# Kernel tuning notes

Measured on AMD Instinct MI355X. Metric: run time of the kernel, lower is better.

The kernel has to match this reference:

```python
import jax, jax.numpy as jnp
import numpy as np

B = 2_000_000
INPUT_DIM = 2
HIDDEN = 32
HALF = HIDDEN // 2  # 16
N_BUCKETS = 50


def setup_inputs() -> dict:
    key = jax.random.key(0)
    ks = jax.random.split(key, 8)
    x = jax.random.normal(ks[0], (B, INPUT_DIM), dtype=jnp.float32)
    buckets = jax.random.randint(ks[1], (B,), 0, N_BUCKETS)
    # shared MLP params (Linear stores W as [out,in]; we keep [in,out] for einsum)
    W1 = jax.random.normal(ks[2], (INPUT_DIM, HIDDEN), dtype=jnp.float32) * 0.5
    b1 = jax.random.normal(ks[3], (HIDDEN,), dtype=jnp.float32) * 0.1
    W2 = jax.random.normal(ks[4], (HIDDEN, HALF), dtype=jnp.float32) * 0.2
    b2 = jax.random.normal(ks[5], (HALF,), dtype=jnp.float32) * 0.1
    # per-bucket heads: each Linear(HALF, 1) -> stacked [N_BUCKETS, HALF] + [N_BUCKETS]
    Wh = jax.random.normal(ks[6], (N_BUCKETS, HALF), dtype=jnp.float32) * 0.2
    bh = jax.random.normal(ks[7], (N_BUCKETS,), dtype=jnp.float32) * 0.1
    return {"x": x, "buckets": buckets, "W1": W1, "b1": b1, "W2": W2, "b2": b2, "Wh": Wh, "bh": bh}


def reference(x, buckets, W1, b1, W2, b2, Wh, bh):
    # shared MLP: Linear -> ReLU -> Linear
    h = jax.nn.relu(x @ W1 + b1) @ W2 + b2            # [B, HALF]
    # bucket routing with clamp-to-last for out-of-range ids
    ids = jnp.where(buckets < N_BUCKETS, buckets, N_BUCKETS - 1)  # [B]
    w = Wh[ids]                                        # [B, HALF] gather
    out = jnp.einsum('bd,bd->b', h, w) + bh[ids]       # [B]
    return out
```

## Files before the change

### kernel.cpp

```cpp
#include <hip/hip_runtime.h>

#define NB 50
#define BLOCK 256


__global__ __launch_bounds__(BLOCK) void precompute_kernel(
    const float* __restrict__ W2,
    const float* __restrict__ b2,
    const float* __restrict__ Wh,
    const float* __restrict__ bh,
    float*       __restrict__ ws)
{
    int t = blockIdx.x * BLOCK + threadIdx.x;
    if (t < NB * 32) {
        int id = t >> 5;
        int k  = t & 31;
        float s = 0.f;
        #pragma unroll
        for (int j = 0; j < 16; ++j)
            s = fmaf(W2[(k << 4) + j], Wh[(id << 4) + j], s);
        int h = (id + (id >> 3)) & 7;
        ws[(id << 5) | ((((k >> 2) ^ h) & 7) << 2) | (k & 3)] = s;
    } else if (t < NB * 32 + NB) {
        int id = t - NB * 32;
        float s = bh[id];
        #pragma unroll
        for (int j = 0; j < 16; ++j)
            s = fmaf(b2[j], Wh[(id << 4) + j], s);
        ws[NB * 32 + id] = s;
    }
}

__device__ __forceinline__ float dot4relu(float x0, float x1,
                                          float4 wa, float4 wb, float4 bb,
                                          float4 v, float acc)
{
    float h;
    h = fmaf(x0, wa.x, fmaf(x1, wb.x, bb.x)); h = fmaxf(h, 0.f); acc = fmaf(h, v.x, acc);
    h = fmaf(x0, wa.y, fmaf(x1, wb.y, bb.y)); h = fmaxf(h, 0.f); acc = fmaf(h, v.y, acc);
    h = fmaf(x0, wa.z, fmaf(x1, wb.z, bb.z)); h = fmaxf(h, 0.f); acc = fmaf(h, v.z, acc);
    h = fmaf(x0, wa.w, fmaf(x1, wb.w, bb.w)); h = fmaxf(h, 0.f); acc = fmaf(h, v.w, acc);
    return acc;
}

__global__ __launch_bounds__(BLOCK) void lightwin_kernel(
    const float4* __restrict__ xq,
    const int4*   __restrict__ bq,
    const float*  __restrict__ W1,
    const float*  __restrict__ b1,
    const float4* __restrict__ wsq,
    float4*       __restrict__ outq,
    int nq)
{
    __shared__ float sVc[416 * 4];

    int tid = blockIdx.x * BLOCK + threadIdx.x;
    bool active = tid < nq;

    float4 xa = {}, xb = {};
    int4 ib = {};
    if (active) {
        xa = xq[2 * tid];
        xb = xq[2 * tid + 1];
        ib = bq[tid];
    }

    float4* sq = (float4*)sVc;
    #pragma unroll
    for (int t = threadIdx.x; t < 416; t += BLOCK)
        sq[t] = wsq[t];
    __syncthreads();

    if (!active) return;

    int id0 = ib.x < NB ? ib.x : NB - 1;
    int id1 = ib.y < NB ? ib.y : NB - 1;
    int id2 = ib.z < NB ? ib.z : NB - 1;
    int id3 = ib.w < NB ? ib.w : NB - 1;
    int h0 = (id0 + (id0 >> 3)) & 7;
    int h1 = (id1 + (id1 >> 3)) & 7;
    int h2 = (id2 + (id2 >> 3)) & 7;
    int h3 = (id3 + (id3 >> 3)) & 7;

    const float4* sV4 = (const float4*)sVc;
    const float*  sc  = sVc + NB * 32;
    const float4* W14 = (const float4*)W1;
    const float4* b14 = (const float4*)b1;

    float acc0 = sc[id0];
    float acc1 = sc[id1];
    float acc2 = sc[id2];
    float acc3 = sc[id3];

    #pragma unroll
    for (int kb = 0; kb < 8; ++kb) {
        float4 wa = W14[kb];
        float4 wb = W14[8 + kb];
        float4 bb = b14[kb];
        float4 v0 = sV4[(id0 << 3) | ((kb ^ h0) & 7)];
        float4 v1 = sV4[(id1 << 3) | ((kb ^ h1) & 7)];
        float4 v2 = sV4[(id2 << 3) | ((kb ^ h2) & 7)];
        float4 v3 = sV4[(id3 << 3) | ((kb ^ h3) & 7)];
        acc0 = dot4relu(xa.x, xa.y, wa, wb, bb, v0, acc0);
        acc1 = dot4relu(xa.z, xa.w, wa, wb, bb, v1, acc1);
        acc2 = dot4relu(xb.x, xb.y, wa, wb, bb, v2, acc2);
        acc3 = dot4relu(xb.z, xb.w, wa, wb, bb, v3, acc3);
    }

    float4 o; o.x = acc0; o.y = acc1; o.z = acc2; o.w = acc3;
    outq[tid] = o;
}

extern "C" void kernel_launch(void* const* d_in, const int* in_sizes, int n_in,
                              void* d_out, int out_size, void* d_ws, size_t ws_size,
                              hipStream_t stream) {
    const float* x       = (const float*)d_in[0];
    const int*   buckets = (const int*)d_in[1];
    const float* W1      = (const float*)d_in[2];
    const float* b1      = (const float*)d_in[3];
    const float* W2      = (const float*)d_in[4];
    const float* b2      = (const float*)d_in[5];
    const float* Wh      = (const float*)d_in[6];
    const float* bh      = (const float*)d_in[7];
    float* out = (float*)d_out;
    float* ws  = (float*)d_ws;

    int B  = in_sizes[1];
    int nq = B / 4;

    precompute_kernel<<<(NB * 32 + NB + BLOCK - 1) / BLOCK, BLOCK, 0, stream>>>(
        W2, b2, Wh, bh, ws);

    int grid = (nq + BLOCK - 1) / BLOCK;
    lightwin_kernel<<<grid, BLOCK, 0, stream>>>(
        (const float4*)x, (const int4*)buckets, W1, b1,
        (const float4*)ws, (float4*)out, nq);
}
```

Before: 89.86 us.

## Use packed fp16 math and fdot2 for hidden layer and head dot products

Converts W1, b1 and the fused W2·Wh head weights to packed half2 in the precompute kernel. The main kernel now computes the hidden activations with packed fp16 FMA and max, and accumulates with fdot2 into fp32. The shared-memory table is re-laid out as [k2][id] with half2 entries, which halves its size and drops the XOR swizzle. This aims to cut VALU instruction count, but fp16 rounding of inputs and weights adds precision risk.

```diff
diff --git a/kernel.cpp b/kernel.cpp
--- a/kernel.cpp
+++ b/kernel.cpp
@@ -4,55 +4,84 @@
 #define BLOCK 256
 
 
+typedef _Float16 hvec2 __attribute__((ext_vector_type(2)));
+
+union h2bits { unsigned u; hvec2 h; };
+
+__device__ __forceinline__ hvec2 u2h2(unsigned u) {
+    h2bits c; c.u = u; return c.h;
+}
+
+__device__ __forceinline__ float dot2acc(hvec2 a, hvec2 b, float c) {
+#if __has_builtin(__builtin_amdgcn_fdot2)
+    return __builtin_amdgcn_fdot2(a, b, c, false);
+#else
+    return fmaf((float)a.x, (float)b.x, fmaf((float)a.y, (float)b.y, c));
+#endif
+}
+
 __global__ __launch_bounds__(BLOCK) void precompute_kernel(
+    const float* __restrict__ W1,
+    const float* __restrict__ b1,
     const float* __restrict__ W2,
     const float* __restrict__ b2,
     const float* __restrict__ Wh,
     const float* __restrict__ bh,
-    float*       __restrict__ ws)
+    unsigned*    __restrict__ ws)
 {
     int t = blockIdx.x * BLOCK + threadIdx.x;
-    if (t < NB * 32) {
-        int id = t >> 5;
-        int k  = t & 31;
-        float s = 0.f;
-        #pragma unroll
-        for (int j = 0; j < 16; ++j)
-            s = fmaf(W2[(k << 4) + j], Wh[(id << 4) + j], s);
-        int h = (id + (id >> 3)) & 7;
-        ws[(id << 5) | ((((k >> 2) ^ h) & 7) << 2) | (k & 3)] = s;
-    } else if (t < NB * 32 + NB) {
-        int id = t - NB * 32;
-        float s = bh[id];
-        #pragma unroll
-        for (int j = 0; j < 16; ++j)
-            s = fmaf(b2[j], Wh[(id << 4) + j], s);
-        ws[NB * 32 + id] = s;
+    if (t < 1024) {
+        int k2 = t >> 6;
+        int id = t & 63;
+        unsigned bits = 0u;
+        if (id < NB) {
+            float f0 = 0.f, f1 = 0.f;
+            int k0 = 2 * k2, k1 = 2 * k2 + 1;
+            #pragma unroll
+            for (int j = 0; j < 16; ++j) {
+                f0 = fmaf(W2[(k0 << 4) + j], Wh[(id << 4) + j], f0);
+                f1 = fmaf(W2[(k1 << 4) + j], Wh[(id << 4) + j], f1);
+            }
+            h2bits c;
+            c.h.x = (_Float16)f0;
+            c.h.y = (_Float16)f1;
+            bits = c.u;
+        }
+        ws[t] = bits;
+    } else if (t < 1088) {
+        int id = t - 1024;
+        unsigned bits = 0u;
+        if (id < NB) {
+            float s = bh[id];
+            #pragma unroll
+            for (int j = 0; j < 16; ++j)
+                s = fmaf(b2[j], Wh[(id << 4) + j], s);
+            bits = __float_as_uint(s);
+        }
+        ws[t] = bits;
+    } else if (t < 1136) {
+        int i = t - 1088;
+        int plane = i >> 4;
+        int k2 = i & 15;
+        float f0, f1;
+        if (plane == 0)      { f0 = W1[2 * k2];      f1 = W1[2 * k2 + 1]; }
+        else if (plane == 1) { f0 = W1[32 + 2 * k2]; f1 = W1[32 + 2 * k2 + 1]; }
+        else                 { f0 = b1[2 * k2];      f1 = b1[2 * k2 + 1]; }
+        h2bits c;
+        c.h.x = (_Float16)f0;
+        c.h.y = (_Float16)f1;
+        ws[t] = c.u;
     }
 }
 
-__device__ __forceinline__ float dot4relu(float x0, float x1,
-                                          float4 wa, float4 wb, float4 bb,
-                                          float4 v, float acc)
-{
-    float h;
-    h = fmaf(x0, wa.x, fmaf(x1, wb.x, bb.x)); h = fmaxf(h, 0.f); acc = fmaf(h, v.x, acc);
-    h = fmaf(x0, wa.y, fmaf(x1, wb.y, bb.y)); h = fmaxf(h, 0.f); acc = fmaf(h, v.y, acc);
-    h = fmaf(x0, wa.z, fmaf(x1, wb.z, bb.z)); h = fmaxf(h, 0.f); acc = fmaf(h, v.z, acc);
-    h = fmaf(x0, wa.w, fmaf(x1, wb.w, bb.w)); h = fmaxf(h, 0.f); acc = fmaf(h, v.w, acc);
-    return acc;
-}
-
 __global__ __launch_bounds__(BLOCK) void lightwin_kernel(
-    const float4* __restrict__ xq,
-    const int4*   __restrict__ bq,
-    const float*  __restrict__ W1,
-    const float*  __restrict__ b1,
-    const float4* __restrict__ wsq,
-    float4*       __restrict__ outq,
+    const float4*   __restrict__ xq,
+    const int4*     __restrict__ bq,
+    const unsigned* __restrict__ wsu,
+    float4*         __restrict__ outq,
     int nq)
 {
-    __shared__ float sVc[416 * 4];
+    __shared__ unsigned sU[1088];
 
     int tid = blockIdx.x * BLOCK + threadIdx.x;
     bool active = tid < nq;
@@ -65,46 +94,49 @@
         ib = bq[tid];
     }
 
-    float4* sq = (float4*)sVc;
-    #pragma unroll
-    for (int t = threadIdx.x; t < 416; t += BLOCK)
-        sq[t] = wsq[t];
+    {
+        float4* sq = (float4*)sU;
+        const float4* wq = (const float4*)wsu;
+        for (int t = threadIdx.x; t < 272; t += BLOCK)
+            sq[t] = wq[t];
+    }
     __syncthreads();
-
     if (!active) return;
 
     int id0 = ib.x < NB ? ib.x : NB - 1;
     int id1 = ib.y < NB ? ib.y : NB - 1;
     int id2 = ib.z < NB ? ib.z : NB - 1;
     int id3 = ib.w < NB ? ib.w : NB - 1;
-    int h0 = (id0 + (id0 >> 3)) & 7;
-    int h1 = (id1 + (id1 >> 3)) & 7;
-    int h2 = (id2 + (id2 >> 3)) & 7;
-    int h3 = (id3 + (id3 >> 3)) & 7;
 
-    const float4* sV4 = (const float4*)sVc;
-    const float*  sc  = sVc + NB * 32;
-    const float4* W14 = (const float4*)W1;
-    const float4* b14 = (const float4*)b1;
+    float acc0 = __uint_as_float(sU[1024 + id0]);
+    float acc1 = __uint_as_float(sU[1024 + id1]);
+    float acc2 = __uint_as_float(sU[1024 + id2]);
+    float acc3 = __uint_as_float(sU[1024 + id3]);
 
-    float acc0 = sc[id0];
-    float acc1 = sc[id1];
-    float acc2 = sc[id2];
-    float acc3 = sc[id3];
+    #define SPLAT2(f) (hvec2){(_Float16)(f), (_Float16)(f)}
+    hvec2 x0e0 = SPLAT2(xa.x), x1e0 = SPLAT2(xa.y);
+    hvec2 x0e1 = SPLAT2(xa.z), x1e1 = SPLAT2(xa.w);
+    hvec2 x0e2 = SPLAT2(xb.x), x1e2 = SPLAT2(xb.y);
+    hvec2 x0e3 = SPLAT2(xb.z), x1e3 = SPLAT2(xb.w);
+    const hvec2 z2 = (hvec2)0;
+
+    const unsigned* wp0 = wsu + 1088;
+    const unsigned* wp1 = wsu + 1104;
+    const unsigned* wpb = wsu + 1120;
 
     #pragma unroll
-    for (int kb = 0; kb < 8; ++kb) {
-        float4 wa = W14[kb];
-        float4 wb = W14[8 + kb];
-        float4 bb = b14[kb];
-        float4 v0 = sV4[(id0 << 3) | ((kb ^ h0) & 7)];
-        float4 v1 = sV4[(id1 << 3) | ((kb ^ h1) & 7)];
-        float4 v2 = sV4[(id2 << 3) | ((kb ^ h2) & 7)];
-        float4 v3 = sV4[(id3 << 3) | ((kb ^ h3) & 7)];
-        acc0 = dot4relu(xa.x, xa.y, wa, wb, bb, v0, acc0);
-        acc1 = dot4relu(xa.z, xa.w, wa, wb, bb, v1, acc1);
-        acc2 = dot4relu(xb.x, xb.y, wa, wb, bb, v2, acc2);
-        acc3 = dot4relu(xb.z, xb.w, wa, wb, bb, v3, acc3);
+    for (int k2 = 0; k2 < 16; ++k2) {
+        hvec2 w0 = u2h2(wp0[k2]);
+        hvec2 w1 = u2h2(wp1[k2]);
+        hvec2 bb = u2h2(wpb[k2]);
+        hvec2 h0 = __builtin_elementwise_max(x0e0 * w0 + x1e0 * w1 + bb, z2);
+        hvec2 h1 = __builtin_elementwise_max(x0e1 * w0 + x1e1 * w1 + bb, z2);
+        hvec2 h2 = __builtin_elementwise_max(x0e2 * w0 + x1e2 * w1 + bb, z2);
+        hvec2 h3 = __builtin_elementwise_max(x0e3 * w0 + x1e3 * w1 + bb, z2);
+        acc0 = dot2acc(h0, u2h2(sU[(k2 << 6) + id0]), acc0);
+        acc1 = dot2acc(h1, u2h2(sU[(k2 << 6) + id1]), acc1);
+        acc2 = dot2acc(h2, u2h2(sU[(k2 << 6) + id2]), acc2);
+        acc3 = dot2acc(h3, u2h2(sU[(k2 << 6) + id3]), acc3);
     }
 
     float4 o; o.x = acc0; o.y = acc1; o.z = acc2; o.w = acc3;
@@ -123,16 +155,15 @@
     const float* Wh      = (const float*)d_in[6];
     const float* bh      = (const float*)d_in[7];
     float* out = (float*)d_out;
-    float* ws  = (float*)d_ws;
+    unsigned* ws = (unsigned*)d_ws;
 
     int B  = in_sizes[1];
     int nq = B / 4;
 
-    precompute_kernel<<<(NB * 32 + NB + BLOCK - 1) / BLOCK, BLOCK, 0, stream>>>(
-        W2, b2, Wh, bh, ws);
+    precompute_kernel<<<(1136 + BLOCK - 1) / BLOCK, BLOCK, 0, stream>>>(
+        W1, b1, W2, b2, Wh, bh, ws);
 
     int grid = (nq + BLOCK - 1) / BLOCK;
     lightwin_kernel<<<grid, BLOCK, 0, stream>>>(
-        (const float4*)x, (const int4*)buckets, W1, b1,
-        (const float4*)ws, (float4*)out, nq);
+        (const float4*)x, (const int4*)buckets, ws, (float4*)out, nq);
 }
```

Result: no change. 89.83 us (-0.0%).
